# Optimization experiments

Hardware: AMD Instinct MI355X
Metric: run time of the kernel (lower is better)

## Reference

```python
import jax, jax.numpy as jnp
import numpy as np
from jax import lax

_MAX_SQRT_GRADIENT = 1000.0
B, T, W, LRU_W, H, TW = 32, 2048, 512, 512, 8, 4


@jax.custom_vjp
def sqrt_bound(x):
    return jnp.sqrt(x)

def _sb_fwd(x):
    return jnp.sqrt(x), x

def _sb_bwd(x, g):
    return (g / jnp.sqrt(jnp.clip(4.0 * x, 1.0 / _MAX_SQRT_GRADIENT ** 2)),)

sqrt_bound.defvjp(_sb_fwd, _sb_bwd)


def setup_inputs() -> dict:
    key = jax.random.key(0)
    ks = jax.random.split(key, 8)
    bw = LRU_W // H
    # RG-LRU `A` parameter: uniform on ring [0.9, 0.999], softplus-inverse transform
    rng = np.random.default_rng(0)
    u = rng.uniform(0.9 ** 2 + 1e-8, 0.999 ** 2 + 1e-8, size=(LRU_W,))
    log_a = 0.5 * np.log(u)
    a_param = np.log(np.exp(-log_a) - 1.0).astype(np.float32)
    return dict(
        x=jax.random.normal(ks[0], (B, T, W), jnp.float32),
        reset=jnp.zeros((B, T), jnp.bool_),
        h0=jnp.zeros((B, LRU_W), jnp.float32),
        w_x=jax.random.normal(ks[1], (W, LRU_W), jnp.float32) / np.sqrt(W).astype(np.float32),
        b_x=jnp.zeros((LRU_W,), jnp.float32),
        w_y=jax.random.normal(ks[2], (W, LRU_W), jnp.float32) / np.sqrt(W).astype(np.float32),
        b_y=jnp.zeros((LRU_W,), jnp.float32),
        conv_w=jax.random.normal(ks[3], (TW, LRU_W), jnp.float32) * np.sqrt(0.01 / TW).astype(np.float32),
        conv_b=jnp.zeros((LRU_W,), jnp.float32),
        a_param=jnp.asarray(a_param),
        wi=jax.random.normal(ks[4], (H, bw, bw), jnp.float32) / np.sqrt(bw).astype(np.float32),
        bi=jnp.zeros((H, bw), jnp.float32),
        wa=jax.random.normal(ks[5], (H, bw, bw), jnp.float32) / np.sqrt(bw).astype(np.float32),
        ba=jnp.zeros((H, bw), jnp.float32),
        w_out=jax.random.normal(ks[6], (LRU_W, W), jnp.float32) / np.sqrt(LRU_W).astype(np.float32),
        b_out=jnp.zeros((W,), jnp.float32),
    )


def _block_diag(x, w, b):
    # x: [B,T,(h*i)] ; w: [h,i,j] ; b: [h,j]
    h, bw, _ = w.shape
    xh = x.reshape(x.shape[:-1] + (h, bw))
    y = jnp.einsum('bthi,hij->bthj', xh, w) + b
    return y.reshape(x.shape[:-1] + (h * bw,))


def _causal_conv1d(x, w, b):
    # output[t] = sum_s w[s] * x[t - (TW-1-s)] + b  (left zero-padded)
    tw = w.shape[0]
    t = x.shape[1]
    xp = jnp.pad(x, ((0, 0), (tw - 1, 0), (0, 0)))
    out = jnp.broadcast_to(b, x.shape).astype(x.dtype)
    for s in range(tw):
        out = out + xp[:, s:s + t] * w[s]
    return out


def _forward(x, reset, h0, w_x, b_x, w_y, b_y, conv_w, conv_b, a_param,
             wi, bi, wa, ba, w_out, b_out):
    xb = x @ w_x + b_x                      # [B,T,LRU_W]
    yb = jax.nn.gelu(x @ w_y + b_y)         # tanh-approx gelu, matches torch approximate='tanh'
    xb = _causal_conv1d(xb, conv_w, conv_b)
    # RG-LRU gating
    gate_x = jax.nn.sigmoid(_block_diag(xb, wi, bi))
    gate_a = jax.nn.sigmoid(_block_diag(xb, wa, ba))
    log_a = -8.0 * gate_a * jax.nn.softplus(a_param)
    a = jnp.exp(log_a)
    mult = sqrt_bound(1.0 - jnp.exp(2.0 * log_a))
    mult = jnp.where(reset[..., None], jnp.ones_like(mult), mult)
    normed = xb * gate_x * mult
    a = a * (1.0 - reset[..., None].astype(a.dtype))  # zero `a` at document boundaries

    def step(h, inp):
        a_t, x_t = inp
        h = a_t * h + x_t
        return h, h

    _, ys = lax.scan(step, h0, (jnp.swapaxes(a, 0, 1), jnp.swapaxes(normed, 0, 1)))
    y = jnp.swapaxes(ys, 0, 1)              # [B,T,LRU_W]
    return (y * yb) @ w_out + b_out


def reference(x, reset, h0, w_x, b_x, w_y, b_y, conv_w, conv_b, a_param,
              wi, bi, wa, ba, w_out, b_out):
    return _forward(x, reset, h0, w_x, b_x, w_y, b_y, conv_w, conv_b, a_param,
                    wi, bi, wa, ba, w_out, b_out)
```

## Files before the change

### kernel.cpp

```cpp
#include <hip/hip_runtime.h>

typedef __bf16 bf16x8 __attribute__((ext_vector_type(8)));
typedef float f32x4 __attribute__((ext_vector_type(4)));
typedef unsigned short u16x8 __attribute__((ext_vector_type(8)));
typedef unsigned short u16x4 __attribute__((ext_vector_type(4)));

#define MBY (1ull << 20)

__device__ __forceinline__ unsigned short f2bf(float f) {
  union { float f; unsigned u; } v; v.f = f;
  unsigned r = v.u + 0x7fffu + ((v.u >> 16) & 1u);
  return (unsigned short)(r >> 16);
}
__device__ __forceinline__ float bf2f(unsigned short s) {
  union { unsigned u; float f; } v; v.u = ((unsigned)s) << 16;
  return v.f;
}
__device__ __forceinline__ float fexp(float x) {
  return __builtin_amdgcn_exp2f(x * 1.44269504088896340736f);
}
__device__ __forceinline__ float frcp(float x) {
  return __builtin_amdgcn_rcpf(x);
}
__device__ __forceinline__ void gl2lds16(const void* g, void* l) {
  __builtin_amdgcn_global_load_lds(
      (const __attribute__((address_space(1))) unsigned int*)g,
      (__attribute__((address_space(3))) unsigned int*)l, 16, 0, 0);
}

__global__ void prep_x_kernel(const float* __restrict__ x, unsigned short* __restrict__ xbf) {
  int g = blockIdx.x * 256 + threadIdx.x;
  float4 v = ((const float4*)x)[g];
  u16x4 o;
  o[0] = f2bf(v.x); o[1] = f2bf(v.y); o[2] = f2bf(v.z); o[3] = f2bf(v.w);
  *(u16x4*)(xbf + (size_t)g * 4) = o;
}

__global__ void prep_misc_kernel(const float* __restrict__ wx, const float* __restrict__ wy,
                                 const float* __restrict__ wo,
                                 const float* __restrict__ wi, const float* __restrict__ wa,
                                 const float* __restrict__ a_param,
                                 unsigned short* __restrict__ wxT, unsigned short* __restrict__ wyT,
                                 unsigned short* __restrict__ woT,
                                 unsigned short* __restrict__ wiTH, unsigned short* __restrict__ wiTL,
                                 unsigned short* __restrict__ waTH, unsigned short* __restrict__ waTL,
                                 float* __restrict__ spbuf) {
  int bid = blockIdx.x, tid = threadIdx.x;
  if (bid < 3072) {
    int mat = bid >> 10;
    int g = (bid & 1023) * 256 + tid;
    int n = g & 511, k = g >> 9;
    const float* src = (mat == 0) ? wx : (mat == 1) ? wy : wo;
    unsigned short* dst = (mat == 0) ? wxT : (mat == 1) ? wyT : woT;
    dst[(size_t)n * 512 + k] = f2bf(src[(size_t)k * 512 + n]);
  } else if (bid < 3200) {
    int g = (bid - 3072) * 256 + tid;
    int j = g & 63, i = (g >> 6) & 63, h = g >> 12;
    size_t src = (size_t)h * 4096 + (size_t)i * 64 + j;
    size_t dst = (size_t)h * 4096 + (size_t)j * 64 + i;
    float v = wi[src];
    unsigned short hh = f2bf(v);
    wiTH[dst] = hh; wiTL[dst] = f2bf(v - bf2f(hh));
    v = wa[src];
    hh = f2bf(v);
    waTH[dst] = hh; waTL[dst] = f2bf(v - bf2f(hh));
  } else {
    int g = (bid - 3200) * 256 + tid;
    if (g < 512) {
      float ap = a_param[g];
      spbuf[g] = (ap > 0.f) ? ap + log1pf(expf(-ap)) : log1pf(expf(ap));
    }
  }
}

__global__ __launch_bounds__(256, 2)
void gemm_dual_kernel(const unsigned short* __restrict__ xbf,
                      const unsigned short* __restrict__ wxT,
                      const unsigned short* __restrict__ wyT,
                      const float* __restrict__ bx, const float* __restrict__ by,
                      unsigned short* __restrict__ xbp, unsigned short* __restrict__ ybuf) {
  __shared__ __align__(16) unsigned short As[128 * 32];
  __shared__ __align__(16) unsigned short Bs0[128 * 32];
  __shared__ __align__(16) unsigned short Bs1[128 * 32];
  const int tid = threadIdx.x, lane = tid & 63, wv = tid >> 6;
  const int m0 = blockIdx.y * 128, n0 = blockIdx.x * 128;
  const int sr = lane >> 2, sk = (lane & 3) * 8;
  const int wm = (wv >> 1) << 6, wn = (wv & 1) << 6;
  const int fm = lane & 15, fq = lane >> 4;

  f32x4 acc0[4][4], acc1[4][4];
#pragma unroll
  for (int i = 0; i < 4; ++i)
#pragma unroll
    for (int j = 0; j < 4; ++j) {
      acc0[i][j] = f32x4{0.f, 0.f, 0.f, 0.f};
      acc1[i][j] = f32x4{0.f, 0.f, 0.f, 0.f};
    }

  const unsigned short* ga  = xbf + (size_t)(m0 + wv * 32 + sr) * 512 + sk;
  const unsigned short* gb0 = wxT + (size_t)(n0 + wv * 32 + sr) * 512 + sk;
  const unsigned short* gb1 = wyT + (size_t)(n0 + wv * 32 + sr) * 512 + sk;
  unsigned short* lA  = &As [wv * 32 * 32];
  unsigned short* lB0 = &Bs0[wv * 32 * 32];
  unsigned short* lB1 = &Bs1[wv * 32 * 32];

  for (int k0 = 0; k0 < 512; k0 += 32) {
    __syncthreads();
    gl2lds16(ga  + k0,            lA);
    gl2lds16(ga  + k0 + 16 * 512, lA  + 16 * 32);
    gl2lds16(gb0 + k0,            lB0);
    gl2lds16(gb0 + k0 + 16 * 512, lB0 + 16 * 32);
    gl2lds16(gb1 + k0,            lB1);
    gl2lds16(gb1 + k0 + 16 * 512, lB1 + 16 * 32);
    __syncthreads();
    bf16x8 af[4], bfr0[4], bfr1[4];
#pragma unroll
    for (int i = 0; i < 4; ++i)
      af[i] = *(const bf16x8*)&As[(wm + i * 16 + fm) * 32 + fq * 8];
#pragma unroll
    for (int j = 0; j < 4; ++j) {
      bfr0[j] = *(const bf16x8*)&Bs0[(wn + j * 16 + fm) * 32 + fq * 8];
      bfr1[j] = *(const bf16x8*)&Bs1[(wn + j * 16 + fm) * 32 + fq * 8];
    }
#pragma unroll
    for (int i = 0; i < 4; ++i)
#pragma unroll
      for (int j = 0; j < 4; ++j) {
        acc0[i][j] = __builtin_amdgcn_mfma_f32_16x16x32_bf16(af[i], bfr0[j], acc0[i][j], 0, 0, 0);
        acc1[i][j] = __builtin_amdgcn_mfma_f32_16x16x32_bf16(af[i], bfr1[j], acc1[i][j], 0, 0, 0);
      }
  }
#pragma unroll
  for (int i = 0; i < 4; ++i) {
#pragma unroll
    for (int j = 0; j < 4; ++j) {
      int col = n0 + wn + j * 16 + fm;
      float bxv = bx[col], byv = by[col];
#pragma unroll
      for (int r = 0; r < 4; ++r) {
        int row = m0 + wm + i * 16 + fq * 4 + r;
        size_t idx = (size_t)row * 512 + col;
        xbp[idx] = f2bf(acc0[i][j][r] + bxv);
        float z = acc1[i][j][r] + byv;
        float zc = 0.7978845608028654f * (z + 0.044715f * z * z * z);
        float e = fexp(2.0f * zc);
        float th = 1.0f - 2.0f * frcp(e + 1.0f);
        ybuf[idx] = f2bf(0.5f * z * (1.0f + th));
      }
    }
  }
}

#define XP 72
__global__ __launch_bounds__(256, 2)
void conv_gates_kernel(const unsigned short* __restrict__ xbp,
                       const unsigned char* __restrict__ reset,
                       const float* __restrict__ conv_w, const float* __restrict__ conv_b,
                       const float* __restrict__ spbuf,
                       const unsigned short* __restrict__ wiTH, const unsigned short* __restrict__ wiTL,
                       const unsigned short* __restrict__ waTH, const unsigned short* __restrict__ waTL,
                       const float* __restrict__ bi, const float* __restrict__ ba,
                       unsigned short* __restrict__ aq_out, unsigned short* __restrict__ nrm) {
  __shared__ __align__(16) unsigned short xin[131 * 64];
  __shared__ __align__(16) unsigned short xcH[128 * XP];
  __shared__ __align__(16) unsigned short xcL[128 * XP];
  const int tile = blockIdx.x, h = blockIdx.y, b = blockIdx.z;
  const int t0 = tile << 7;
  const int tid = threadIdx.x, lane = tid & 63, wv = tid >> 6;
  const int fm = lane & 15, fq = lane >> 4;

  const size_t cb0 = ((size_t)b * 2048) * 512 + (h << 6);
  for (int idx = tid; idx < 1048; idx += 256) {
    int row = idx >> 3, c8 = (idx & 7) << 3;
    int t = t0 - 3 + row;
    u16x8 v = u16x8{0, 0, 0, 0, 0, 0, 0, 0};
    if (t >= 0) v = *(const u16x8*)(xbp + cb0 + (size_t)t * 512 + c8);
    *(u16x8*)&xin[row * 64 + c8] = v;
  }
  __syncthreads();
  {
    const int c8 = (tid & 7) << 3, u0 = tid >> 3;
    const int ch8 = (h << 6) + c8;
    float cw[4][8], cbv[8];
#pragma unroll
    for (int s = 0; s < 4; ++s) {
      *(float4*)&cw[s][0] = *(const float4*)(conv_w + s * 512 + ch8);
      *(float4*)&cw[s][4] = *(const float4*)(conv_w + s * 512 + ch8 + 4);
    }
    *(float4*)&cbv[0] = *(const float4*)(conv_b + ch8);
    *(float4*)&cbv[4] = *(const float4*)(conv_b + ch8 + 4);
#pragma unroll
    for (int g = 0; g < 4; ++g) {
      int u = u0 + g * 32;
      u16x8 r0 = *(const u16x8*)&xin[(u + 0) * 64 + c8];
      u16x8 r1 = *(const u16x8*)&xin[(u + 1) * 64 + c8];
      u16x8 r2 = *(const u16x8*)&xin[(u + 2) * 64 + c8];
      u16x8 r3 = *(const u16x8*)&xin[(u + 3) * 64 + c8];
      u16x8 oh, ol;
#pragma unroll
      for (int j = 0; j < 8; ++j) {
        float v = cbv[j] + cw[0][j] * bf2f(r0[j]) + cw[1][j] * bf2f(r1[j]) +
                  cw[2][j] * bf2f(r2[j]) + cw[3][j] * bf2f(r3[j]);
        oh[j] = f2bf(v);
        ol[j] = f2bf(v - bf2f(oh[j]));
      }
      *(u16x8*)&xcH[u * XP + c8] = oh;
      *(u16x8*)&xcL[u * XP + c8] = ol;
    }
  }
  bf16x8 bIh[4][2], bIl[4][2], bAh[4][2], bAl[4][2];
#pragma unroll
  for (int nt = 0; nt < 4; ++nt)
#pragma unroll
    for (int ks = 0; ks < 2; ++ks) {
      size_t off = (size_t)h * 4096 + (size_t)(nt * 16 + fm) * 64 + ks * 32 + fq * 8;
      bIh[nt][ks] = *(const bf16x8*)(wiTH + off);
      bIl[nt][ks] = *(const bf16x8*)(wiTL + off);
      bAh[nt][ks] = *(const bf16x8*)(waTH + off);
      bAl[nt][ks] = *(const bf16x8*)(waTL + off);
    }
  f32x4 accI[2][4], accA[2][4];
#pragma unroll
  for (int mt = 0; mt < 2; ++mt)
#pragma unroll
    for (int nt = 0; nt < 4; ++nt) {
      accI[mt][nt] = f32x4{0.f, 0.f, 0.f, 0.f};
      accA[mt][nt] = f32x4{0.f, 0.f, 0.f, 0.f};
    }
  __syncthreads();
#pragma unroll
  for (int mt = 0; mt < 2; ++mt) {
    int mrow = wv * 32 + mt * 16 + fm;
#pragma unroll
    for (int ks = 0; ks < 2; ++ks) {
      bf16x8 ah = *(const bf16x8*)&xcH[mrow * XP + ks * 32 + fq * 8];
      bf16x8 al = *(const bf16x8*)&xcL[mrow * XP + ks * 32 + fq * 8];
#pragma unroll
      for (int nt = 0; nt < 4; ++nt) {
        accI[mt][nt] = __builtin_amdgcn_mfma_f32_16x16x32_bf16(ah, bIh[nt][ks], accI[mt][nt], 0, 0, 0);
        accI[mt][nt] = __builtin_amdgcn_mfma_f32_16x16x32_bf16(ah, bIl[nt][ks], accI[mt][nt], 0, 0, 0);
        accI[mt][nt] = __builtin_amdgcn_mfma_f32_16x16x32_bf16(al, bIh[nt][ks], accI[mt][nt], 0, 0, 0);
        accA[mt][nt] = __builtin_amdgcn_mfma_f32_16x16x32_bf16(ah, bAh[nt][ks], accA[mt][nt], 0, 0, 0);
        accA[mt][nt] = __builtin_amdgcn_mfma_f32_16x16x32_bf16(ah, bAl[nt][ks], accA[mt][nt], 0, 0, 0);
        accA[mt][nt] = __builtin_amdgcn_mfma_f32_16x16x32_bf16(al, bAh[nt][ks], accA[mt][nt], 0, 0, 0);
      }
    }
  }
#pragma unroll
  for (int nt = 0; nt < 4; ++nt) {
    int colg = (h << 6) + nt * 16 + fm;
    float biv = bi[colg], bav = ba[colg];
    float sp8 = -8.0f * spbuf[colg];
#pragma unroll
    for (int mt = 0; mt < 2; ++mt) {
#pragma unroll
      for (int r = 0; r < 4; ++r) {
        int mrow = wv * 32 + mt * 16 + fq * 4 + r;
        int t = t0 + mrow;
        float xcv = bf2f(xcH[mrow * XP + nt * 16 + fm]) + bf2f(xcL[mrow * XP + nt * 16 + fm]);
        float gx = frcp(1.0f + fexp(-(accI[mt][nt][r] + biv)));
        float ga = frcp(1.0f + fexp(-(accA[mt][nt][r] + bav)));
        float la = sp8 * ga;
        float av = fexp(la);
        float mult = __builtin_amdgcn_sqrtf(fmaxf(1.0f - fexp(2.0f * la), 0.0f));
        if (reset[b * 2048 + t]) { mult = 1.0f; av = 0.0f; }
        size_t idx = ((size_t)(b * 2048 + t)) * 512 + colg;
        aq_out[idx] = (unsigned short)fminf(av * 65536.0f + 0.5f, 65535.0f);
        nrm[idx] = f2bf(xcv * gx * mult);
      }
    }
  }
}

__global__ void scan1_kernel(const unsigned short* __restrict__ aq, const unsigned short* __restrict__ nrm,
                             float* __restrict__ cA, float* __restrict__ cH) {
  int g = blockIdx.x * 256 + threadIdx.x;
  int c4 = (g & 127) << 2, k = (g >> 7) & 31, b = g >> 12;
  size_t base = ((size_t)(b * 2048 + k * 64)) * 512 + c4;
  float A[4] = {1.f, 1.f, 1.f, 1.f}, h[4] = {0.f, 0.f, 0.f, 0.f};
#pragma unroll 4
  for (int i = 0; i < 64; ++i) {
    u16x4 av = *(const u16x4*)(aq + base + (size_t)i * 512);
    u16x4 nv = *(const u16x4*)(nrm + base + (size_t)i * 512);
#pragma unroll
    for (int j = 0; j < 4; ++j) {
      float a = (float)av[j] * (1.0f / 65536.0f);
      A[j] *= a;
      h[j] = fmaf(a, h[j], bf2f(nv[j]));
    }
  }
  int ci = ((b * 32 + k) << 9) + c4;
#pragma unroll
  for (int j = 0; j < 4; ++j) { cA[ci + j] = A[j]; cH[ci + j] = h[j]; }
}

__global__ void scan2_kernel(const float* __restrict__ cA, const float* __restrict__ cH,
                             const float* __restrict__ h0, float* __restrict__ hinit) {
  int b = blockIdx.x, c = threadIdx.x;
  float h = h0[b * 512 + c];
  for (int k = 0; k < 32; ++k) {
    int ci = ((b * 32 + k) << 9) + c;
    hinit[ci] = h;
    h = fmaf(cA[ci], h, cH[ci]);
  }
}

__global__ void scan3_kernel(const unsigned short* __restrict__ aq, const unsigned short* __restrict__ nrm,
                             const float* __restrict__ hinit, const unsigned short* __restrict__ ybuf,
                             unsigned short* __restrict__ p) {
  int g = blockIdx.x * 256 + threadIdx.x;
  int c4 = (g & 127) << 2, k = (g >> 7) & 31, b = g >> 12;
  size_t base = ((size_t)(b * 2048 + k * 64)) * 512 + c4;
  int ci = ((b * 32 + k) << 9) + c4;
  float h[4];
#pragma unroll
  for (int j = 0; j < 4; ++j) h[j] = hinit[ci + j];
#pragma unroll 4
  for (int i = 0; i < 64; ++i) {
    u16x4 av = *(const u16x4*)(aq + base + (size_t)i * 512);
    u16x4 nv = *(const u16x4*)(nrm + base + (size_t)i * 512);
    u16x4 yv = *(const u16x4*)(ybuf + base + (size_t)i * 512);
    u16x4 pv;
#pragma unroll
    for (int j = 0; j < 4; ++j) {
      float a = (float)av[j] * (1.0f / 65536.0f);
      h[j] = fmaf(a, h[j], bf2f(nv[j]));
      pv[j] = f2bf(h[j] * bf2f(yv[j]));
    }
    *(u16x4*)(p + base + (size_t)i * 512) = pv;
  }
}

__global__ __launch_bounds__(256, 2)
void gemm_out_kernel(const unsigned short* __restrict__ p,
                     const unsigned short* __restrict__ woT,
                     const float* __restrict__ bout, float* __restrict__ out) {
  __shared__ __align__(16) unsigned short As[128 * 32];
  __shared__ __align__(16) unsigned short Bs[128 * 32];
  const int tid = threadIdx.x, lane = tid & 63, wv = tid >> 6;
  const int m0 = blockIdx.y * 128, n0 = blockIdx.x * 128;
  const int sr = lane >> 2, sk = (lane & 3) * 8;
  const int wm = (wv >> 1) << 6, wn = (wv & 1) << 6;
  const int fm = lane & 15, fq = lane >> 4;

  f32x4 acc[4][4];
#pragma unroll
  for (int i = 0; i < 4; ++i)
#pragma unroll
    for (int j = 0; j < 4; ++j) acc[i][j] = f32x4{0.f, 0.f, 0.f, 0.f};

  const unsigned short* ga = p   + (size_t)(m0 + wv * 32 + sr) * 512 + sk;
  const unsigned short* gb = woT + (size_t)(n0 + wv * 32 + sr) * 512 + sk;
  unsigned short* lA = &As[wv * 32 * 32];
  unsigned short* lB = &Bs[wv * 32 * 32];

  for (int k0 = 0; k0 < 512; k0 += 32) {
    __syncthreads();
    gl2lds16(ga + k0,            lA);
    gl2lds16(ga + k0 + 16 * 512, lA + 16 * 32);
    gl2lds16(gb + k0,            lB);
    gl2lds16(gb + k0 + 16 * 512, lB + 16 * 32);
    __syncthreads();
    bf16x8 af[4], bfr[4];
#pragma unroll
    for (int i = 0; i < 4; ++i)
      af[i] = *(const bf16x8*)&As[(wm + i * 16 + fm) * 32 + fq * 8];
#pragma unroll
    for (int j = 0; j < 4; ++j)
      bfr[j] = *(const bf16x8*)&Bs[(wn + j * 16 + fm) * 32 + fq * 8];
#pragma unroll
    for (int i = 0; i < 4; ++i)
#pragma unroll
      for (int j = 0; j < 4; ++j)
        acc[i][j] = __builtin_amdgcn_mfma_f32_16x16x32_bf16(af[i], bfr[j], acc[i][j], 0, 0, 0);
  }
#pragma unroll
  for (int i = 0; i < 4; ++i) {
#pragma unroll
    for (int j = 0; j < 4; ++j) {
      int col = n0 + wn + j * 16 + fm;
      float bv = bout[col];
#pragma unroll
      for (int r = 0; r < 4; ++r) {
        int row = m0 + wm + i * 16 + fq * 4 + r;
        out[(size_t)row * 512 + col] = acc[i][j][r] + bv;
      }
    }
  }
}

extern "C" void kernel_launch(void* const* d_in, const int* in_sizes, int n_in,
                              void* d_out, int out_size, void* d_ws, size_t ws_size,
                              hipStream_t stream) {
  const float* x             = (const float*)d_in[0];
  const unsigned char* reset = (const unsigned char*)d_in[1];
  const float* h0            = (const float*)d_in[2];
  const float* b_x           = (const float*)d_in[4];
  const float* b_y           = (const float*)d_in[6];
  const float* conv_w        = (const float*)d_in[7];
  const float* conv_b        = (const float*)d_in[8];
  const float* bi            = (const float*)d_in[11];
  const float* ba            = (const float*)d_in[13];
  const float* b_out         = (const float*)d_in[15];

  char* ws = (char*)d_ws;
  unsigned short* xbp  = (unsigned short*)(ws);
  unsigned short* ybuf = (unsigned short*)(ws + 64 * MBY);
  unsigned short* aq   = (unsigned short*)(ws + 128 * MBY);
  unsigned short* nrm  = (unsigned short*)(ws + 192 * MBY);
  unsigned short* xbf  = (unsigned short*)(ws + 192 * MBY);
  float* cA            = (float*)(ws + 256 * MBY);
  float* cH            = (float*)(ws + 258 * MBY);
  float* hinit         = (float*)(ws + 260 * MBY);
  unsigned short* wxT  = (unsigned short*)(ws + 262 * MBY);
  unsigned short* wyT  = (unsigned short*)(ws + 262 * MBY + 524288);
  unsigned short* woT  = (unsigned short*)(ws + 263 * MBY);
  unsigned short* wiTH = (unsigned short*)(ws + 263 * MBY + 524288);
  unsigned short* wiTL = wiTH + 32768;
  unsigned short* waTH = wiTL + 32768;
  unsigned short* waTL = waTH + 32768;
  float* spbuf         = (float*)(waTL + 32768);
  unsigned short* p    = xbp;

  hipLaunchKernelGGL(prep_x_kernel, dim3(32768), dim3(256), 0, stream, x, xbf);
  hipLaunchKernelGGL(prep_misc_kernel, dim3(3202), dim3(256), 0, stream,
                     (const float*)d_in[3], (const float*)d_in[5], (const float*)d_in[14],
                     (const float*)d_in[10], (const float*)d_in[12], (const float*)d_in[9],
                     wxT, wyT, woT, wiTH, wiTL, waTH, waTL, spbuf);
  hipLaunchKernelGGL(gemm_dual_kernel, dim3(4, 512), dim3(256), 0, stream,
                     xbf, wxT, wyT, b_x, b_y, xbp, ybuf);
  hipLaunchKernelGGL(conv_gates_kernel, dim3(16, 8, 32), dim3(256), 0, stream,
                     xbp, reset, conv_w, conv_b, spbuf, wiTH, wiTL, waTH, waTL,
                     bi, ba, aq, nrm);
  hipLaunchKernelGGL(scan1_kernel, dim3(512), dim3(256), 0, stream, aq, nrm, cA, cH);
  hipLaunchKernelGGL(scan2_kernel, dim3(32), dim3(512), 0, stream, cA, cH, h0, hinit);
  hipLaunchKernelGGL(scan3_kernel, dim3(512), dim3(256), 0, stream, aq, nrm, hinit, ybuf, p);
  hipLaunchKernelGGL(gemm_out_kernel, dim3(4, 512), dim3(256), 0, stream, p, woT, b_out, (float*)d_out);
}
```

Baseline: 606.6 us.

## Fuse scan chunk-reduction into conv_gates kernel and alias LDS buffers

Removes the separate scan1 kernel by having each conv_gates block compute the per-64-step chunk products and partial states for its own tile after writing aq/nrm. The xin staging buffer is aliased with xcH, with an extra barrier and register staging, to shrink LDS so launch bounds can target 4 blocks per SM. The intent is to save a launch and improve occupancy. In exchange, only 128 threads read back the freshly written global data through scalar strided loads, leaving the other threads idle during that tail.

```diff
diff --git a/kernel.cpp b/kernel.cpp
--- a/kernel.cpp
+++ b/kernel.cpp
@@ -152,7 +152,7 @@
 }
 
 #define XP 72
-__global__ __launch_bounds__(256, 2)
+__global__ __launch_bounds__(256, 4)
 void conv_gates_kernel(const unsigned short* __restrict__ xbp,
                        const unsigned char* __restrict__ reset,
                        const float* __restrict__ conv_w, const float* __restrict__ conv_b,
@@ -160,10 +160,12 @@
                        const unsigned short* __restrict__ wiTH, const unsigned short* __restrict__ wiTL,
                        const unsigned short* __restrict__ waTH, const unsigned short* __restrict__ waTL,
                        const float* __restrict__ bi, const float* __restrict__ ba,
-                       unsigned short* __restrict__ aq_out, unsigned short* __restrict__ nrm) {
-  __shared__ __align__(16) unsigned short xin[131 * 64];
-  __shared__ __align__(16) unsigned short xcH[128 * XP];
-  __shared__ __align__(16) unsigned short xcL[128 * XP];
+                       unsigned short* __restrict__ aq_out, unsigned short* __restrict__ nrm,
+                       float* __restrict__ cA, float* __restrict__ cH) {
+  __shared__ __align__(16) unsigned short lds[2 * 128 * XP];
+  unsigned short* xin = lds;
+  unsigned short* xcH = lds;
+  unsigned short* xcL = lds + 128 * XP;
   const int tile = blockIdx.x, h = blockIdx.y, b = blockIdx.z;
   const int t0 = tile << 7;
   const int tid = threadIdx.x, lane = tid & 63, wv = tid >> 6;
@@ -178,9 +180,10 @@
     *(u16x8*)&xin[row * 64 + c8] = v;
   }
   __syncthreads();
+  u16x8 ohr[4], olr[4];
+  const int cc8 = (tid & 7) << 3, u0 = tid >> 3;
   {
-    const int c8 = (tid & 7) << 3, u0 = tid >> 3;
-    const int ch8 = (h << 6) + c8;
+    const int ch8 = (h << 6) + cc8;
     float cw[4][8], cbv[8];
 #pragma unroll
     for (int s = 0; s < 4; ++s) {
@@ -192,10 +195,10 @@
 #pragma unroll
     for (int g = 0; g < 4; ++g) {
       int u = u0 + g * 32;
-      u16x8 r0 = *(const u16x8*)&xin[(u + 0) * 64 + c8];
-      u16x8 r1 = *(const u16x8*)&xin[(u + 1) * 64 + c8];
-      u16x8 r2 = *(const u16x8*)&xin[(u + 2) * 64 + c8];
-      u16x8 r3 = *(const u16x8*)&xin[(u + 3) * 64 + c8];
+      u16x8 r0 = *(const u16x8*)&xin[(u + 0) * 64 + cc8];
+      u16x8 r1 = *(const u16x8*)&xin[(u + 1) * 64 + cc8];
+      u16x8 r2 = *(const u16x8*)&xin[(u + 2) * 64 + cc8];
+      u16x8 r3 = *(const u16x8*)&xin[(u + 3) * 64 + cc8];
       u16x8 oh, ol;
 #pragma unroll
       for (int j = 0; j < 8; ++j) {
@@ -204,9 +207,15 @@
         oh[j] = f2bf(v);
         ol[j] = f2bf(v - bf2f(oh[j]));
       }
-      *(u16x8*)&xcH[u * XP + c8] = oh;
-      *(u16x8*)&xcL[u * XP + c8] = ol;
-    }
+      ohr[g] = oh; olr[g] = ol;
+    }
+  }
+  __syncthreads();
+#pragma unroll
+  for (int g = 0; g < 4; ++g) {
+    int u = u0 + g * 32;
+    *(u16x8*)&xcH[u * XP + cc8] = ohr[g];
+    *(u16x8*)&xcL[u * XP + cc8] = olr[g];
   }
   bf16x8 bIh[4][2], bIl[4][2], bAh[4][2], bAl[4][2];
 #pragma unroll
@@ -270,28 +279,20 @@
       }
     }
   }
-}
-
-__global__ void scan1_kernel(const unsigned short* __restrict__ aq, const unsigned short* __restrict__ nrm,
-                             float* __restrict__ cA, float* __restrict__ cH) {
-  int g = blockIdx.x * 256 + threadIdx.x;
-  int c4 = (g & 127) << 2, k = (g >> 7) & 31, b = g >> 12;
-  size_t base = ((size_t)(b * 2048 + k * 64)) * 512 + c4;
-  float A[4] = {1.f, 1.f, 1.f, 1.f}, h[4] = {0.f, 0.f, 0.f, 0.f};
+  __syncthreads();
+  if (tid < 128) {
+    const int kk = tid >> 6, ch = tid & 63;
+    const size_t base = ((size_t)(b * 2048 + t0 + kk * 64)) * 512 + (h << 6) + ch;
+    float A = 1.f, hacc = 0.f;
 #pragma unroll 4
-  for (int i = 0; i < 64; ++i) {
-    u16x4 av = *(const u16x4*)(aq + base + (size_t)i * 512);
-    u16x4 nv = *(const u16x4*)(nrm + base + (size_t)i * 512);
-#pragma unroll
-    for (int j = 0; j < 4; ++j) {
-      float a = (float)av[j] * (1.0f / 65536.0f);
-      A[j] *= a;
-      h[j] = fmaf(a, h[j], bf2f(nv[j]));
-    }
-  }
-  int ci = ((b * 32 + k) << 9) + c4;
-#pragma unroll
-  for (int j = 0; j < 4; ++j) { cA[ci + j] = A[j]; cH[ci + j] = h[j]; }
+    for (int i = 0; i < 64; ++i) {
+      float a = (float)aq_out[base + (size_t)i * 512] * (1.0f / 65536.0f);
+      A *= a;
+      hacc = fmaf(a, hacc, bf2f(nrm[base + (size_t)i * 512]));
+    }
+    const int ci = ((b * 32 + (tile << 1) + kk) << 9) + (h << 6) + ch;
+    cA[ci] = A; cH[ci] = hacc;
+  }
 }
 
 __global__ void scan2_kernel(const float* __restrict__ cA, const float* __restrict__ cH,
@@ -431,8 +432,7 @@
                      xbf, wxT, wyT, b_x, b_y, xbp, ybuf);
   hipLaunchKernelGGL(conv_gates_kernel, dim3(16, 8, 32), dim3(256), 0, stream,
                      xbp, reset, conv_w, conv_b, spbuf, wiTH, wiTL, waTH, waTL,
-                     bi, ba, aq, nrm);
-  hipLaunchKernelGGL(scan1_kernel, dim3(512), dim3(256), 0, stream, aq, nrm, cA, cH);
+                     bi, ba, aq, nrm, cA, cH);
   hipLaunchKernelGGL(scan2_kernel, dim3(32), dim3(512), 0, stream, cA, cH, h0, hinit);
   hipLaunchKernelGGL(scan3_kernel, dim3(512), dim3(256), 0, stream, aq, nrm, hinit, ybuf, p);
   hipLaunchKernelGGL(gemm_out_kernel, dim3(4, 512), dim3(256), 0, stream, p, woT, b_out, (float*)d_out);
```

Result: slower. 720.1 us (+18.7%).
